# Optimization experiments

Hardware: AMD Instinct MI355X
Metric: run time of the kernel (lower is better)

Reference implementation:

```python
import jax, jax.numpy as jnp
import numpy as np

N_HEADS = 16
NEG = -1e9


def setup_inputs() -> dict:
    key = jax.random.key(0)
    ks = jax.random.split(key, 6)
    B, S, D = 4, 2048, 2048
    scale = 1.0 / np.sqrt(D)
    x = jax.random.normal(ks[0], (B, S, D), dtype=jnp.float32)
    attention_mask = jax.random.randint(ks[1], (B, S), 0, 2, dtype=jnp.int32)
    w_q = jax.random.normal(ks[2], (D, D), dtype=jnp.float32) * scale
    w_k = jax.random.normal(ks[3], (D, D), dtype=jnp.float32) * scale
    w_v = jax.random.normal(ks[4], (D, D), dtype=jnp.float32) * scale
    w_o = jax.random.normal(ks[5], (D, D), dtype=jnp.float32) * scale
    return {"x": x, "attention_mask": attention_mask,
            "w_q": w_q, "w_k": w_k, "w_v": w_v, "w_o": w_o}


def reference(x, attention_mask, w_q, w_k, w_v, w_o):
    B, S, D = x.shape
    H = N_HEADS
    dk = D // H

    def split_heads(t):  # [B,S,D] -> [B,H,S,dk]
        return t.reshape(B, S, H, dk).transpose(0, 2, 1, 3)

    # torch nn.Linear: y = x @ W.T (no bias)
    q = split_heads(x @ w_q.T)
    k = split_heads(x @ w_k.T)
    v = split_heads(x @ w_v.T)

    scores = jnp.einsum('bhqd,bhkd->bhqk', q, k) / jnp.sqrt(jnp.float32(dk))
    # padding mask over keys: [B,1,1,S]
    pad = attention_mask[:, None, None, :] != 0
    scores = jnp.where(pad, scores, NEG)
    # causal mask
    causal = jnp.tril(jnp.ones((S, S), dtype=bool))
    scores = jnp.where(causal[None, None, :, :], scores, NEG)

    attn = jax.nn.softmax(scores, axis=-1)
    # dropout p=0.0 -> identity
    out = jnp.einsum('bhqk,bhkd->bhqd', attn, v)
    out = out.transpose(0, 2, 1, 3).reshape(B, S, D)
    return out @ w_o.T
```

## Files before the change

### kernel.cpp

```cpp
#include <hip/hip_runtime.h>

typedef __bf16 bf16;
typedef __bf16 bf16x4 __attribute__((ext_vector_type(4)));
typedef __bf16 bf16x8 __attribute__((ext_vector_type(8)));
typedef float f32x4 __attribute__((ext_vector_type(4)));

#define NEGF (-1e9f)

__device__ __forceinline__ void gload16(const void* g, void* l) {
  __builtin_amdgcn_global_load_lds(
      (__attribute__((address_space(1))) void*)(void*)g,
      (__attribute__((address_space(3))) void*)l, 16, 0, 0);
}

__global__ __launch_bounds__(256)
void prep_kernel(const float* __restrict__ x, const int* __restrict__ mask,
                 const float* __restrict__ wq, const float* __restrict__ wk,
                 const float* __restrict__ wv, const float* __restrict__ wo,
                 bf16* __restrict__ xb, bf16* __restrict__ wqb,
                 bf16* __restrict__ wkb, bf16* __restrict__ wvb,
                 bf16* __restrict__ wob, float* __restrict__ maskadd,
                 int* __restrict__ firstone)
{
  const float QS = 1.44269504f * 0.08838834764f;
  const size_t i = ((size_t)blockIdx.x * 256 + threadIdx.x) * 4;
  if (i < (size_t)16777216) {
    const float4 v = *(const float4*)&x[i];
    bf16x4 o4 = {(bf16)v.x, (bf16)v.y, (bf16)v.z, (bf16)v.w};
    *(bf16x4*)&xb[i] = o4;
  }
  if (i < (size_t)4194304) {
    float4 v = *(const float4*)&wq[i];
    bf16x4 o4 = {(bf16)(v.x * QS), (bf16)(v.y * QS), (bf16)(v.z * QS), (bf16)(v.w * QS)};
    *(bf16x4*)&wqb[i] = o4;
    v = *(const float4*)&wk[i];
    bf16x4 o5 = {(bf16)v.x, (bf16)v.y, (bf16)v.z, (bf16)v.w};
    *(bf16x4*)&wkb[i] = o5;
    v = *(const float4*)&wv[i];
    bf16x4 o6 = {(bf16)v.x, (bf16)v.y, (bf16)v.z, (bf16)v.w};
    *(bf16x4*)&wvb[i] = o6;
    v = *(const float4*)&wo[i];
    bf16x4 o7 = {(bf16)v.x, (bf16)v.y, (bf16)v.z, (bf16)v.w};
    *(bf16x4*)&wob[i] = o7;
  }
  if (i < (size_t)8192) {
    const int4 m4 = *(const int4*)&mask[i];
    float4 o4 = {m4.x ? 0.f : NEGF, m4.y ? 0.f : NEGF,
                 m4.z ? 0.f : NEGF, m4.w ? 0.f : NEGF};
    *(float4*)&maskadd[i] = o4;
  }
  if (blockIdx.x == 16383) {
    __shared__ int fm;
    for (int b = 0; b < 4; ++b) {
      if (threadIdx.x == 0) fm = 2048;
      __syncthreads();
      int lm = 2048;
      for (int s = threadIdx.x; s < 2048; s += 256)
        if (mask[(b << 11) + s] != 0) lm = min(lm, s);
      atomicMin(&fm, lm);
      __syncthreads();
      if (threadIdx.x == 0) firstone[b] = fm;
      __syncthreads();
    }
  }
}

__device__ __forceinline__ void gemm_core128(
    const bf16* __restrict__ A, const bf16* __restrict__ Bt, int K,
    int rowBase, int colBase, bf16* As, bf16* Bs, f32x4 acc[4][4])
{
  const int t = threadIdx.x;
  const int lane = t & 63;
  const int w = t >> 6;
  const int wm = (w >> 1) << 6;
  const int wn = (w & 1) << 6;
  const int l15 = lane & 15;
  const int quad = lane >> 4;

  for (int k0 = 0; k0 < K; k0 += 64) {
    __syncthreads();
#pragma unroll
    for (int i = 0; i < 4; ++i) {
      const int c = (i << 8) + t;
      const int row = c >> 3;
      const int col = ((c & 7) ^ (row & 7)) << 3;
      gload16(&A[(size_t)(rowBase + row) * K + k0 + col], &As[c << 3]);
    }
#pragma unroll
    for (int i = 0; i < 4; ++i) {
      const int c = (i << 8) + t;
      const int row = c >> 3;
      const int col = ((c & 7) ^ (row & 7)) << 3;
      gload16(&Bt[(size_t)(colBase + row) * K + k0 + col], &Bs[c << 3]);
    }
    __syncthreads();
#pragma unroll
    for (int ks = 0; ks < 2; ++ks) {
      bf16x8 a[4], b[4];
#pragma unroll
      for (int mi = 0; mi < 4; ++mi) {
        const int row = wm + (mi << 4) + l15;
        a[mi] = *(const bf16x8*)&As[(row << 6) + ((((ks << 2) + quad) ^ (row & 7)) << 3)];
      }
#pragma unroll
      for (int ni = 0; ni < 4; ++ni) {
        const int row = wn + (ni << 4) + l15;
        b[ni] = *(const bf16x8*)&Bs[(row << 6) + ((((ks << 2) + quad) ^ (row & 7)) << 3)];
      }
#pragma unroll
      for (int mi = 0; mi < 4; ++mi)
#pragma unroll
        for (int ni = 0; ni < 4; ++ni)
          acc[mi][ni] = __builtin_amdgcn_mfma_f32_16x16x32_bf16(
              a[mi], b[ni], acc[mi][ni], 0, 0, 0);
    }
  }
}

__global__ __launch_bounds__(256, 2)
void qkv_gemm_kernel(const bf16* __restrict__ xb,
                     const bf16* __restrict__ wqb, const bf16* __restrict__ wkb,
                     const bf16* __restrict__ wvb,
                     bf16* __restrict__ qb, bf16* __restrict__ kb,
                     bf16* __restrict__ vtb)
{
  __shared__ __align__(16) bf16 As[128 * 64];
  __shared__ __align__(16) bf16 Bs[128 * 64];
  const int z = blockIdx.z;
  const bf16* Bt = (z == 0) ? wqb : (z == 1) ? wkb : wvb;
  bf16* dst = (z == 0) ? qb : (z == 1) ? kb : vtb;
  const int rowBase = blockIdx.y << 7;
  const int colBase = blockIdx.x << 7;
  f32x4 acc[4][4];
#pragma unroll
  for (int mi = 0; mi < 4; ++mi)
#pragma unroll
    for (int ni = 0; ni < 4; ++ni)
#pragma unroll
      for (int r = 0; r < 4; ++r) acc[mi][ni][r] = 0.f;

  gemm_core128(xb, Bt, 2048, rowBase, colBase, As, Bs, acc);

  const int lane = threadIdx.x & 63;
  const int w = threadIdx.x >> 6;
  const int wm = (w >> 1) << 6;
  const int wn = (w & 1) << 6;
  const int l15 = lane & 15;
  const int quad = lane >> 4;
#pragma unroll
  for (int mi = 0; mi < 4; ++mi)
#pragma unroll
    for (int ni = 0; ni < 4; ++ni)
#pragma unroll
      for (int r = 0; r < 4; ++r) {
        const int row = rowBase + wm + (mi << 4) + (quad << 2) + r;
        const int col = colBase + wn + (ni << 4) + l15;
        const int b = row >> 11, s = row & 2047;
        const int h = col >> 7, d = col & 127;
        const bf16 v = (bf16)acc[mi][ni][r];
        if (z == 2) dst[((((b << 4) + h) << 7) + d) * 2048 + s] = v;
        else        dst[(((((b << 4) + h) << 11) + s) << 7) + d] = v;
      }
}

__global__ __launch_bounds__(256, 2)
void out_gemm_kernel(const bf16* __restrict__ attnb, const bf16* __restrict__ wob,
                     float* __restrict__ out)
{
  __shared__ __align__(16) bf16 As[128 * 64];
  __shared__ __align__(16) bf16 Bs[128 * 64];
  const int rowBase = blockIdx.y << 7;
  const int colBase = blockIdx.x << 7;
  f32x4 acc[4][4];
#pragma unroll
  for (int mi = 0; mi < 4; ++mi)
#pragma unroll
    for (int ni = 0; ni < 4; ++ni)
#pragma unroll
      for (int r = 0; r < 4; ++r) acc[mi][ni][r] = 0.f;

  gemm_core128(attnb, wob, 2048, rowBase, colBase, As, Bs, acc);

  const int lane = threadIdx.x & 63;
  const int w = threadIdx.x >> 6;
  const int wm = (w >> 1) << 6;
  const int wn = (w & 1) << 6;
  const int l15 = lane & 15;
  const int quad = lane >> 4;
#pragma unroll
  for (int mi = 0; mi < 4; ++mi)
#pragma unroll
    for (int ni = 0; ni < 4; ++ni)
#pragma unroll
      for (int r = 0; r < 4; ++r) {
        const int row = rowBase + wm + (mi << 4) + (quad << 2) + r;
        const int col = colBase + wn + (ni << 4) + l15;
        out[((size_t)row << 11) + col] = acc[mi][ni][r];
      }
}

__global__ __launch_bounds__(256, 2)
void flash_kernel(const bf16* __restrict__ qb, const bf16* __restrict__ kb,
                  const bf16* __restrict__ vtb, const float* __restrict__ maskadd,
                  bf16* __restrict__ attnb)
{
  __shared__ __align__(16) bf16 Ks[64 * 128];
  __shared__ __align__(16) bf16 Vs[128 * 64];

  const int h = blockIdx.y, b = blockIdx.z;
  const int qt = (b & 1) ? (int)blockIdx.x : 15 - (int)blockIdx.x;
  const int t = threadIdx.x, lane = t & 63, w = t >> 6;
  const int quad = lane >> 4, l15 = lane & 15;
  const int bh = (b << 4) + h;
  const bf16* Qp = qb + (size_t)bh * (2048 * 128);
  const bf16* Kp = kb + (size_t)bh * (2048 * 128);
  const bf16* Vp = vtb + (size_t)bh * (128 * 2048);
  const int qrow0 = (qt << 7) + (w << 5);

  bf16x8 qf[2][4];
#pragma unroll
  for (int mi = 0; mi < 2; ++mi)
#pragma unroll
    for (int kk = 0; kk < 4; ++kk)
      qf[mi][kk] = *(const bf16x8*)&Qp[((qrow0 + (mi << 4) + l15) << 7) + (kk << 5) + (quad << 3)];

  f32x4 o[2][8];
  float lpart[2][4];
#pragma unroll
  for (int mi = 0; mi < 2; ++mi)
#pragma unroll
    for (int r = 0; r < 4; ++r) lpart[mi][r] = 0.f;
#pragma unroll
  for (int mi = 0; mi < 2; ++mi)
#pragma unroll
    for (int dj = 0; dj < 8; ++dj)
#pragma unroll
      for (int r = 0; r < 4; ++r) o[mi][dj][r] = 0.f;

  bf16* Pw = &Ks[w << 11];
  const int nkt = (qt << 1) + 2;
  for (int kt = 0; kt < nkt; ++kt) {
    __syncthreads();
#pragma unroll
    for (int i = 0; i < 4; ++i) {
      const int c = (i << 8) + t;
      const int row = c >> 4;
      const int col = ((c & 15) ^ (row & 15)) << 3;
      gload16(&Kp[(((kt << 6) + row) << 7) + col], &Ks[c << 3]);
    }
#pragma unroll
    for (int i = 0; i < 4; ++i) {
      const int c = (i << 8) + t;
      const int row = c >> 3;
      const int col = ((c & 7) ^ (row & 7)) << 3;
      gload16(&Vp[(row << 11) + (kt << 6) + col], &Vs[c << 3]);
    }
    __syncthreads();

    const bool skip = (kt << 6) > qrow0 + 31;
    f32x4 S[2][4];
    if (!skip) {
#pragma unroll
      for (int mi = 0; mi < 2; ++mi)
#pragma unroll
        for (int nj = 0; nj < 4; ++nj)
#pragma unroll
          for (int r = 0; r < 4; ++r) S[mi][nj][r] = 0.f;
#pragma unroll
      for (int kk = 0; kk < 4; ++kk) {
        bf16x8 kf[4];
#pragma unroll
        for (int nj = 0; nj < 4; ++nj) {
          const int key = (nj << 4) + l15;
          const int gd = (kk << 2) + quad;
          kf[nj] = *(const bf16x8*)&Ks[(key << 7) + ((gd ^ (key & 15)) << 3)];
        }
#pragma unroll
        for (int mi = 0; mi < 2; ++mi)
#pragma unroll
          for (int nj = 0; nj < 4; ++nj)
            S[mi][nj] = __builtin_amdgcn_mfma_f32_16x16x32_bf16(qf[mi][kk], kf[nj], S[mi][nj], 0, 0, 0);
      }
      float mv[4];
#pragma unroll
      for (int nj = 0; nj < 4; ++nj)
        mv[nj] = maskadd[(b << 11) + (kt << 6) + (nj << 4) + l15];
      const bool diag = ((kt << 6) + 63 > qrow0);
#pragma unroll
      for (int mi = 0; mi < 2; ++mi)
#pragma unroll
        for (int nj = 0; nj < 4; ++nj)
#pragma unroll
          for (int r = 0; r < 4; ++r) {
            float s = S[mi][nj][r] + mv[nj];
            if (diag) {
              const int key = (kt << 6) + (nj << 4) + l15;
              const int qrow = qrow0 + (mi << 4) + (quad << 2) + r;
              if (key > qrow) s += NEGF;
            }
            const float p = __builtin_amdgcn_exp2f(s);
            S[mi][nj][r] = p;
            lpart[mi][r] += p;
          }
    }
    __syncthreads();
    if (!skip) {
#pragma unroll
      for (int mi = 0; mi < 2; ++mi)
#pragma unroll
        for (int nj = 0; nj < 4; ++nj)
#pragma unroll
          for (int r = 0; r < 4; ++r) {
            const int row = (mi << 4) + (quad << 2) + r;
            const int col = (nj << 4) + l15;
            Pw[(row << 6) + ((((col >> 3) ^ (row & 7)) << 3) | (col & 7))] = (bf16)S[mi][nj][r];
          }
#pragma unroll
      for (int kk = 0; kk < 2; ++kk) {
        bf16x8 pf[2];
#pragma unroll
        for (int mi = 0; mi < 2; ++mi) {
          const int row = (mi << 4) + l15;
          pf[mi] = *(const bf16x8*)&Pw[(row << 6) + ((((kk << 2) + quad) ^ (row & 7)) << 3)];
        }
#pragma unroll
        for (int dj = 0; dj < 8; ++dj) {
          const int d = (dj << 4) + l15;
          const int gd = (kk << 2) + quad;
          const bf16x8 vf = *(const bf16x8*)&Vs[(d << 6) + ((gd ^ (d & 7)) << 3)];
#pragma unroll
          for (int mi = 0; mi < 2; ++mi)
            o[mi][dj] = __builtin_amdgcn_mfma_f32_16x16x32_bf16(pf[mi], vf, o[mi][dj], 0, 0, 0);
        }
      }
    }
  }

#pragma unroll
  for (int mi = 0; mi < 2; ++mi)
#pragma unroll
    for (int r = 0; r < 4; ++r) {
      float s = lpart[mi][r];
#pragma unroll
      for (int off = 1; off < 16; off <<= 1) s += __shfl_xor(s, off);
      const float inv = 1.0f / s;
      const int row = qrow0 + (mi << 4) + (quad << 2) + r;
#pragma unroll
      for (int dj = 0; dj < 8; ++dj) {
        const int d = (dj << 4) + l15;
        attnb[((size_t)((b << 11) + row) << 11) + (h << 7) + d] = (bf16)(o[mi][dj][r] * inv);
      }
    }
}

__global__ void mean_v_kernel(const bf16* __restrict__ vtb, float* __restrict__ meanv)
{
  const int row = blockIdx.x;
  float sum = 0.f;
  for (int s = threadIdx.x; s < 2048; s += 256)
    sum += (float)vtb[((size_t)row << 11) + s];
#pragma unroll
  for (int off = 1; off < 64; off <<= 1) sum += __shfl_xor(sum, off);
  __shared__ float part[4];
  if ((threadIdx.x & 63) == 0) part[threadIdx.x >> 6] = sum;
  __syncthreads();
  if (threadIdx.x == 0)
    meanv[row] = (part[0] + part[1] + part[2] + part[3]) * (1.0f / 2048.0f);
}

__global__ void fixup_kernel(const int* __restrict__ firstone,
                             const float* __restrict__ meanv,
                             bf16* __restrict__ attnb)
{
  const int b = blockIdx.x, h = blockIdx.y, d = threadIdx.x;
  const int f = firstone[b];
  const bf16 v = (bf16)meanv[(((b << 4) + h) << 7) + d];
  for (int s = 0; s < f; ++s)
    attnb[((size_t)((b << 11) + s) << 11) + (h << 7) + d] = v;
}

extern "C" void kernel_launch(void* const* d_in, const int* in_sizes, int n_in,
                              void* d_out, int out_size, void* d_ws, size_t ws_size,
                              hipStream_t stream)
{
  const float* x  = (const float*)d_in[0];
  const int* mask = (const int*)d_in[1];
  const float* wq = (const float*)d_in[2];
  const float* wk = (const float*)d_in[3];
  const float* wv = (const float*)d_in[4];
  const float* wo = (const float*)d_in[5];
  float* out = (float*)d_out;

  char* ws = (char*)d_ws;
  bf16* xb      = (bf16*)(ws + 0);
  bf16* wqb     = (bf16*)(ws + 33554432);
  bf16* wkb     = (bf16*)(ws + 41943040);
  bf16* wvb     = (bf16*)(ws + 50331648);
  bf16* wob     = (bf16*)(ws + 58720256);
  bf16* qb      = (bf16*)(ws + 67108864);
  bf16* kb      = (bf16*)(ws + 100663296);
  bf16* vtb     = (bf16*)(ws + 134217728);
  bf16* attnb   = (bf16*)(ws + 167772160);
  float* maskadd= (float*)(ws + 201326592);
  float* meanv  = (float*)(ws + 201359360);
  int* firstone = (int*)(ws + 201392128);

  prep_kernel<<<16384, 256, 0, stream>>>(x, mask, wq, wk, wv, wo,
                                         xb, wqb, wkb, wvb, wob, maskadd, firstone);
  qkv_gemm_kernel<<<dim3(16, 64, 3), 256, 0, stream>>>(xb, wqb, wkb, wvb, qb, kb, vtb);
  mean_v_kernel<<<8192, 256, 0, stream>>>(vtb, meanv);
  flash_kernel<<<dim3(16, 16, 4), 256, 0, stream>>>(qb, kb, vtb, maskadd, attnb);
  fixup_kernel<<<dim3(4, 16), 128, 0, stream>>>(firstone, meanv, attnb);
  out_gemm_kernel<<<dim3(16, 64), 256, 0, stream>>>(attnb, wob, out);
}
```

Measured before the change: 599.0 us.

## Double-buffer K/V tiles in flash attention and raise MFMA wave priority

```diff
diff --git a/kernel.cpp b/kernel.cpp
--- a/kernel.cpp
+++ b/kernel.cpp
@@ -204,8 +204,8 @@
                   const bf16* __restrict__ vtb, const float* __restrict__ maskadd,
                   bf16* __restrict__ attnb)
 {
-  __shared__ __align__(16) bf16 Ks[64 * 128];
-  __shared__ __align__(16) bf16 Vs[128 * 64];
+  __shared__ __align__(16) bf16 Ks[2][64 * 128];
+  __shared__ __align__(16) bf16 Vs[2][128 * 64];
 
   const int h = blockIdx.y, b = blockIdx.z;
   const int qt = (b & 1) ? (int)blockIdx.x : 15 - (int)blockIdx.x;
@@ -217,45 +217,53 @@
   const bf16* Vp = vtb + (size_t)bh * (128 * 2048);
   const int qrow0 = (qt << 7) + (w << 5);
 
-  bf16x8 qf[2][4];
-#pragma unroll
-  for (int mi = 0; mi < 2; ++mi)
-#pragma unroll
-    for (int kk = 0; kk < 4; ++kk)
-      qf[mi][kk] = *(const bf16x8*)&Qp[((qrow0 + (mi << 4) + l15) << 7) + (kk << 5) + (quad << 3)];
-
-  f32x4 o[2][8];
-  float lpart[2][4];
-#pragma unroll
-  for (int mi = 0; mi < 2; ++mi)
-#pragma unroll
-    for (int r = 0; r < 4; ++r) lpart[mi][r] = 0.f;
-#pragma unroll
-  for (int mi = 0; mi < 2; ++mi)
-#pragma unroll
-    for (int dj = 0; dj < 8; ++dj)
-#pragma unroll
-      for (int r = 0; r < 4; ++r) o[mi][dj][r] = 0.f;
-
-  bf16* Pw = &Ks[w << 11];
-  const int nkt = (qt << 1) + 2;
-  for (int kt = 0; kt < nkt; ++kt) {
-    __syncthreads();
+  auto stageKV = [&](int buf, int kt) {
 #pragma unroll
     for (int i = 0; i < 4; ++i) {
       const int c = (i << 8) + t;
       const int row = c >> 4;
       const int col = ((c & 15) ^ (row & 15)) << 3;
-      gload16(&Kp[(((kt << 6) + row) << 7) + col], &Ks[c << 3]);
+      gload16(&Kp[(((kt << 6) + row) << 7) + col], &Ks[buf][c << 3]);
     }
 #pragma unroll
     for (int i = 0; i < 4; ++i) {
       const int c = (i << 8) + t;
       const int row = c >> 3;
       const int col = ((c & 7) ^ (row & 7)) << 3;
-      gload16(&Vp[(row << 11) + (kt << 6) + col], &Vs[c << 3]);
-    }
-    __syncthreads();
+      gload16(&Vp[(row << 11) + (kt << 6) + col], &Vs[buf][c << 3]);
+    }
+  };
+
+  stageKV(0, 0);
+
+  bf16x8 qf[2][4];
+#pragma unroll
+  for (int mi = 0; mi < 2; ++mi)
+#pragma unroll
+    for (int kk = 0; kk < 4; ++kk)
+      qf[mi][kk] = *(const bf16x8*)&Qp[((qrow0 + (mi << 4) + l15) << 7) + (kk << 5) + (quad << 3)];
+
+  f32x4 o[2][8];
+  float lpart[2][4];
+#pragma unroll
+  for (int mi = 0; mi < 2; ++mi)
+#pragma unroll
+    for (int r = 0; r < 4; ++r) lpart[mi][r] = 0.f;
+#pragma unroll
+  for (int mi = 0; mi < 2; ++mi)
+#pragma unroll
+    for (int dj = 0; dj < 8; ++dj)
+#pragma unroll
+      for (int r = 0; r < 4; ++r) o[mi][dj][r] = 0.f;
+
+  asm volatile("s_waitcnt vmcnt(0)" ::: "memory");
+  __builtin_amdgcn_s_barrier();
+  asm volatile("" ::: "memory");
+
+  const int nkt = (qt << 1) + 2;
+  for (int kt = 0; kt < nkt; ++kt) {
+    const int cur = kt & 1;
+    if (kt + 1 < nkt) stageKV(cur ^ 1, kt + 1);
 
     const bool skip = (kt << 6) > qrow0 + 31;
     f32x4 S[2][4];
@@ -266,6 +274,7 @@
         for (int nj = 0; nj < 4; ++nj)
 #pragma unroll
           for (int r = 0; r < 4; ++r) S[mi][nj][r] = 0.f;
+      __builtin_amdgcn_s_setprio(1);
 #pragma unroll
       for (int kk = 0; kk < 4; ++kk) {
         bf16x8 kf[4];
@@ -273,7 +282,7 @@
         for (int nj = 0; nj < 4; ++nj) {
           const int key = (nj << 4) + l15;
           const int gd = (kk << 2) + quad;
-          kf[nj] = *(const bf16x8*)&Ks[(key << 7) + ((gd ^ (key & 15)) << 3)];
+          kf[nj] = *(const bf16x8*)&Ks[cur][(key << 7) + ((gd ^ (key & 15)) << 3)];
         }
 #pragma unroll
         for (int mi = 0; mi < 2; ++mi)
@@ -281,6 +290,7 @@
           for (int nj = 0; nj < 4; ++nj)
             S[mi][nj] = __builtin_amdgcn_mfma_f32_16x16x32_bf16(qf[mi][kk], kf[nj], S[mi][nj], 0, 0, 0);
       }
+      __builtin_amdgcn_s_setprio(0);
       float mv[4];
 #pragma unroll
       for (int nj = 0; nj < 4; ++nj)
@@ -303,8 +313,11 @@
             lpart[mi][r] += p;
           }
     }
-    __syncthreads();
+    asm volatile("" ::: "memory");
+    __builtin_amdgcn_s_barrier();
+    asm volatile("" ::: "memory");
     if (!skip) {
+      bf16* Pw = &Ks[cur][w << 11];
 #pragma unroll
       for (int mi = 0; mi < 2; ++mi)
 #pragma unroll
@@ -323,17 +336,22 @@
           const int row = (mi << 4) + l15;
           pf[mi] = *(const bf16x8*)&Pw[(row << 6) + ((((kk << 2) + quad) ^ (row & 7)) << 3)];
         }
+        __builtin_amdgcn_s_setprio(1);
 #pragma unroll
         for (int dj = 0; dj < 8; ++dj) {
           const int d = (dj << 4) + l15;
           const int gd = (kk << 2) + quad;
-          const bf16x8 vf = *(const bf16x8*)&Vs[(d << 6) + ((gd ^ (d & 7)) << 3)];
+          const bf16x8 vf = *(const bf16x8*)&Vs[cur][(d << 6) + ((gd ^ (d & 7)) << 3)];
 #pragma unroll
           for (int mi = 0; mi < 2; ++mi)
             o[mi][dj] = __builtin_amdgcn_mfma_f32_16x16x32_bf16(pf[mi], vf, o[mi][dj], 0, 0, 0);
         }
-      }
-    }
+        __builtin_amdgcn_s_setprio(0);
+      }
+    }
+    asm volatile("s_waitcnt vmcnt(0)" ::: "memory");
+    __builtin_amdgcn_s_barrier();
+    asm volatile("" ::: "memory");
   }
 
 #pragma unroll
```

Result: slower. 634.2 us (+5.9%).

## Rewrite projection GEMMs as 256x256 double-buffered tiles with XCD-aware block remap

Applied to the files above, without the earlier changes.

```diff
diff --git a/kernel.cpp b/kernel.cpp
--- a/kernel.cpp
+++ b/kernel.cpp
@@ -65,96 +65,143 @@
   }
 }
 
-__device__ __forceinline__ void gemm_core128(
-    const bf16* __restrict__ A, const bf16* __restrict__ Bt, int K,
-    int rowBase, int colBase, bf16* As, bf16* Bs, f32x4 acc[4][4])
-{
+__device__ __forceinline__ void gemm_core256(
+    const bf16* __restrict__ A, const bf16* __restrict__ Bt, const int K,
+    const int rowBase, const int colBase, f32x4 acc[8][4])
+{
+  __shared__ __align__(16) bf16 As[2][256 * 64];
+  __shared__ __align__(16) bf16 Bs[2][256 * 64];
+
   const int t = threadIdx.x;
   const int lane = t & 63;
   const int w = t >> 6;
-  const int wm = (w >> 1) << 6;
-  const int wn = (w & 1) << 6;
+  const int mh = (w >> 2) << 7;
+  const int nq = (w & 3) << 6;
   const int l15 = lane & 15;
   const int quad = lane >> 4;
 
-  for (int k0 = 0; k0 < K; k0 += 64) {
-    __syncthreads();
-#pragma unroll
-    for (int i = 0; i < 4; ++i) {
-      const int c = (i << 8) + t;
-      const int row = c >> 3;
-      const int col = ((c & 7) ^ (row & 7)) << 3;
-      gload16(&A[(size_t)(rowBase + row) * K + k0 + col], &As[c << 3]);
-    }
-#pragma unroll
-    for (int i = 0; i < 4; ++i) {
-      const int c = (i << 8) + t;
-      const int row = c >> 3;
-      const int col = ((c & 7) ^ (row & 7)) << 3;
-      gload16(&Bt[(size_t)(colBase + row) * K + k0 + col], &Bs[c << 3]);
-    }
-    __syncthreads();
-#pragma unroll
-    for (int ks = 0; ks < 2; ++ks) {
-      bf16x8 a[4], b[4];
-#pragma unroll
-      for (int mi = 0; mi < 4; ++mi) {
-        const int row = wm + (mi << 4) + l15;
-        a[mi] = *(const bf16x8*)&As[(row << 6) + ((((ks << 2) + quad) ^ (row & 7)) << 3)];
-      }
-#pragma unroll
-      for (int ni = 0; ni < 4; ++ni) {
-        const int row = wn + (ni << 4) + l15;
-        b[ni] = *(const bf16x8*)&Bs[(row << 6) + ((((ks << 2) + quad) ^ (row & 7)) << 3)];
-      }
+  const int srow = t >> 3;
+  const int scol = ((t & 7) ^ (srow & 7)) << 3;
+  const int doff = (srow << 6) + ((t & 7) << 3);
+
+  auto issueA = [&](int buf, int k0, int g) {
+    gload16(&A[(size_t)(rowBase + (g << 6) + srow) * K + k0 + scol],
+            &As[buf][(g << 12) + doff]);
+  };
+  auto issueB = [&](int buf, int k0, int g) {
+    gload16(&Bt[(size_t)(colBase + (g << 6) + srow) * K + k0 + scol],
+            &Bs[buf][(g << 12) + doff]);
+  };
+
+  issueB(0, 0, 0); issueB(0, 0, 2); issueB(0, 0, 1); issueB(0, 0, 3);
+  issueA(0, 0, 0); issueA(0, 0, 2); issueA(0, 0, 1); issueA(0, 0, 3);
+
+  const int NT = K >> 6;
+  for (int tt = 0; tt < NT; ++tt) {
+    const int cur = tt & 1;
+    const int nxt = cur ^ 1;
+    const int k1 = (tt + 1 < NT) ? ((tt + 1) << 6) : 0;
+
+    asm volatile("s_waitcnt vmcnt(2)" ::: "memory");
+    __builtin_amdgcn_s_barrier();
+    asm volatile("" ::: "memory");
+    issueB(nxt, k1, 0); issueB(nxt, k1, 2);
+
+    bf16x8 b[4][2], a[4][2];
+#pragma unroll
+    for (int ni = 0; ni < 4; ++ni)
+#pragma unroll
+      for (int ks = 0; ks < 2; ++ks) {
+        const int row = nq + (ni << 4) + l15;
+        b[ni][ks] = *(const bf16x8*)&Bs[cur][(row << 6) + ((((ks << 2) + quad) ^ (row & 7)) << 3)];
+      }
+#pragma unroll
+    for (int mi = 0; mi < 4; ++mi)
+#pragma unroll
+      for (int ks = 0; ks < 2; ++ks) {
+        const int row = mh + (mi << 4) + l15;
+        a[mi][ks] = *(const bf16x8*)&As[cur][(row << 6) + ((((ks << 2) + quad) ^ (row & 7)) << 3)];
+      }
+    __builtin_amdgcn_s_setprio(1);
+#pragma unroll
+    for (int ks = 0; ks < 2; ++ks)
 #pragma unroll
       for (int mi = 0; mi < 4; ++mi)
 #pragma unroll
         for (int ni = 0; ni < 4; ++ni)
           acc[mi][ni] = __builtin_amdgcn_mfma_f32_16x16x32_bf16(
-              a[mi], b[ni], acc[mi][ni], 0, 0, 0);
-    }
-  }
-}
-
-__global__ __launch_bounds__(256, 2)
+              a[mi][ks], b[ni][ks], acc[mi][ni], 0, 0, 0);
+    __builtin_amdgcn_s_setprio(0);
+    issueB(nxt, k1, 1); issueB(nxt, k1, 3);
+
+    asm volatile("s_waitcnt vmcnt(4)" ::: "memory");
+    __builtin_amdgcn_s_barrier();
+    asm volatile("" ::: "memory");
+    issueA(nxt, k1, 0); issueA(nxt, k1, 2);
+#pragma unroll
+    for (int mi = 0; mi < 4; ++mi)
+#pragma unroll
+      for (int ks = 0; ks < 2; ++ks) {
+        const int row = mh + 64 + (mi << 4) + l15;
+        a[mi][ks] = *(const bf16x8*)&As[cur][(row << 6) + ((((ks << 2) + quad) ^ (row & 7)) << 3)];
+      }
+    __builtin_amdgcn_s_setprio(1);
+#pragma unroll
+    for (int ks = 0; ks < 2; ++ks)
+#pragma unroll
+      for (int mi = 0; mi < 4; ++mi)
+#pragma unroll
+        for (int ni = 0; ni < 4; ++ni)
+          acc[mi + 4][ni] = __builtin_amdgcn_mfma_f32_16x16x32_bf16(
+              a[mi][ks], b[ni][ks], acc[mi + 4][ni], 0, 0, 0);
+    __builtin_amdgcn_s_setprio(0);
+    issueA(nxt, k1, 1); issueA(nxt, k1, 3);
+  }
+  asm volatile("s_waitcnt vmcnt(0)" ::: "memory");
+  __builtin_amdgcn_s_barrier();
+  asm volatile("" ::: "memory");
+}
+
+__global__ __launch_bounds__(512, 2)
 void qkv_gemm_kernel(const bf16* __restrict__ xb,
                      const bf16* __restrict__ wqb, const bf16* __restrict__ wkb,
                      const bf16* __restrict__ wvb,
                      bf16* __restrict__ qb, bf16* __restrict__ kb,
                      bf16* __restrict__ vtb)
 {
-  __shared__ __align__(16) bf16 As[128 * 64];
-  __shared__ __align__(16) bf16 Bs[128 * 64];
-  const int z = blockIdx.z;
+  const int id = blockIdx.x;
+  const int nid = ((id & 7) * 96) + (id >> 3);
+  const int z = nid >> 8;
+  const int rem = nid & 255;
+  const int rowBase = (rem >> 3) << 8;
+  const int colBase = (rem & 7) << 8;
   const bf16* Bt = (z == 0) ? wqb : (z == 1) ? wkb : wvb;
   bf16* dst = (z == 0) ? qb : (z == 1) ? kb : vtb;
-  const int rowBase = blockIdx.y << 7;
-  const int colBase = blockIdx.x << 7;
-  f32x4 acc[4][4];
-#pragma unroll
-  for (int mi = 0; mi < 4; ++mi)
+
+  f32x4 acc[8][4];
+#pragma unroll
+  for (int mi = 0; mi < 8; ++mi)
 #pragma unroll
     for (int ni = 0; ni < 4; ++ni)
 #pragma unroll
       for (int r = 0; r < 4; ++r) acc[mi][ni][r] = 0.f;
 
-  gemm_core128(xb, Bt, 2048, rowBase, colBase, As, Bs, acc);
+  gemm_core256(xb, Bt, 2048, rowBase, colBase, acc);
 
   const int lane = threadIdx.x & 63;
   const int w = threadIdx.x >> 6;
-  const int wm = (w >> 1) << 6;
-  const int wn = (w & 1) << 6;
+  const int mh = (w >> 2) << 7;
+  const int nq = (w & 3) << 6;
   const int l15 = lane & 15;
   const int quad = lane >> 4;
 #pragma unroll
-  for (int mi = 0; mi < 4; ++mi)
+  for (int mi = 0; mi < 8; ++mi)
 #pragma unroll
     for (int ni = 0; ni < 4; ++ni)
 #pragma unroll
       for (int r = 0; r < 4; ++r) {
-        const int row = rowBase + wm + (mi << 4) + (quad << 2) + r;
-        const int col = colBase + wn + (ni << 4) + l15;
+        const int row = rowBase + mh + (mi << 4) + (quad << 2) + r;
+        const int col = colBase + nq + (ni << 4) + l15;
         const int b = row >> 11, s = row & 2047;
         const int h = col >> 7, d = col & 127;
         const bf16 v = (bf16)acc[mi][ni][r];
@@ -163,38 +210,39 @@
       }
 }
 
-__global__ __launch_bounds__(256, 2)
+__global__ __launch_bounds__(512, 2)
 void out_gemm_kernel(const bf16* __restrict__ attnb, const bf16* __restrict__ wob,
                      float* __restrict__ out)
 {
-  __shared__ __align__(16) bf16 As[128 * 64];
-  __shared__ __align__(16) bf16 Bs[128 * 64];
-  const int rowBase = blockIdx.y << 7;
-  const int colBase = blockIdx.x << 7;
-  f32x4 acc[4][4];
-#pragma unroll
-  for (int mi = 0; mi < 4; ++mi)
+  const int id = blockIdx.x;
+  const int nid = ((id & 7) * 32) + (id >> 3);
+  const int rowBase = (nid >> 3) << 8;
+  const int colBase = (nid & 7) << 8;
+
+  f32x4 acc[8][4];
+#pragma unroll
+  for (int mi = 0; mi < 8; ++mi)
 #pragma unroll
     for (int ni = 0; ni < 4; ++ni)
 #pragma unroll
       for (int r = 0; r < 4; ++r) acc[mi][ni][r] = 0.f;
 
-  gemm_core128(attnb, wob, 2048, rowBase, colBase, As, Bs, acc);
+  gemm_core256(attnb, wob, 2048, rowBase, colBase, acc);
 
   const int lane = threadIdx.x & 63;
   const int w = threadIdx.x >> 6;
-  const int wm = (w >> 1) << 6;
-  const int wn = (w & 1) << 6;
+  const int mh = (w >> 2) << 7;
+  const int nq = (w & 3) << 6;
   const int l15 = lane & 15;
   const int quad = lane >> 4;
 #pragma unroll
-  for (int mi = 0; mi < 4; ++mi)
+  for (int mi = 0; mi < 8; ++mi)
 #pragma unroll
     for (int ni = 0; ni < 4; ++ni)
 #pragma unroll
       for (int r = 0; r < 4; ++r) {
-        const int row = rowBase + wm + (mi << 4) + (quad << 2) + r;
-        const int col = colBase + wn + (ni << 4) + l15;
+        const int row = rowBase + mh + (mi << 4) + (quad << 2) + r;
+        const int col = colBase + nq + (ni << 4) + l15;
         out[((size_t)row << 11) + col] = acc[mi][ni][r];
       }
 }
@@ -407,9 +455,9 @@
 
   prep_kernel<<<16384, 256, 0, stream>>>(x, mask, wq, wk, wv, wo,
                                          xb, wqb, wkb, wvb, wob, maskadd, firstone);
-  qkv_gemm_kernel<<<dim3(16, 64, 3), 256, 0, stream>>>(xb, wqb, wkb, wvb, qb, kb, vtb);
+  qkv_gemm_kernel<<<768, 512, 0, stream>>>(xb, wqb, wkb, wvb, qb, kb, vtb);
   mean_v_kernel<<<8192, 256, 0, stream>>>(vtb, meanv);
   flash_kernel<<<dim3(16, 16, 4), 256, 0, stream>>>(qb, kb, vtb, maskadd, attnb);
   fixup_kernel<<<dim3(4, 16), 128, 0, stream>>>(firstone, meanv, attnb);
-  out_gemm_kernel<<<dim3(16, 64), 256, 0, stream>>>(attnb, wob, out);
-}
+  out_gemm_kernel<<<256, 512, 0, stream>>>(attnb, wob, out);
+}
```

Result: slower. 689.7 us (+15.1%).
